# Kernel optimization log

Hardware: AMD Instinct MI355X
Metric: run time of the kernel (lower is better)

Reference implementation:

```python
import jax, jax.numpy as jnp
import numpy as np

E = 256   # embed_dim
L = 64    # num_landmarks
C = 256   # in_channels
N_ITER = 6


def iterative_inv(K):
    # Newton-Schulz pseudo-inverse on small [*, L, L] matrices (faithful to torch code)
    I = jnp.eye(K.shape[-1], dtype=K.dtype)
    KA = jnp.abs(K)
    V0 = KA.sum(axis=-2, keepdims=True).max(axis=-1, keepdims=True)  # [*,1,1]
    VI = KA.sum(axis=-1, keepdims=True).max(axis=-2, keepdims=True)  # [*,1,1]
    V = jnp.swapaxes(K, -1, -2) / (V0 * VI)
    for _ in range(N_ITER):
        KV = K @ V
        V = 0.25 * V @ (13.0 * I - KV @ (15.0 * I - KV @ (7.0 * I - KV)))
    return V


def setup_inputs() -> dict:
    key = jax.random.key(0)
    k0, k1, k2 = jax.random.split(key, 3)
    x = jax.random.normal(k0, (8, C, 64, 64), dtype=jnp.float32)
    # Conv2d 1x1 weights stored as [out, in]
    w_qkv = jax.random.normal(k1, (3 * E, C), dtype=jnp.float32) * 0.02
    b_qkv = jnp.zeros((3 * E,), dtype=jnp.float32)
    w_out = jax.random.normal(k2, (C, E), dtype=jnp.float32) * 0.02
    b_out = jnp.zeros((C,), dtype=jnp.float32)
    return {"x": x, "w_qkv": w_qkv, "b_qkv": b_qkv, "w_out": w_out, "b_out": b_out}


def reference(x, w_qkv, b_qkv, w_out, b_out):
    N, Cin, H, W = x.shape
    HW = H * W
    # 1x1 conv: [N, 3E, H, W]
    y = jnp.einsum('nchw,ec->nehw', x, w_qkv) + b_qkv[None, :, None, None]
    # faithful raw reshape (mixes channel/spatial like the torch code)
    qkv = y.reshape(N, HW, 3 * E)
    q, k, v = jnp.split(qkv, 3, axis=-1)                     # each [N, HW, E]
    scale = HW ** 0.5
    q_land = q.reshape(N, L, HW // L, E).mean(axis=-2) / scale  # [N, L, E]
    k_land = k.reshape(N, L, HW // L, E).mean(axis=-2) / scale  # [N, L, E]
    # three softmaxes, all over dim=-2 as in the original
    k1 = jax.nn.softmax(jnp.einsum('nie,nje->nij', q, k_land), axis=-2)       # [N, HW, L]
    k2 = jax.nn.softmax(jnp.einsum('nie,nje->nij', q_land, k_land), axis=-2)  # [N, L, L]
    k3 = jax.nn.softmax(jnp.einsum('nie,nje->nij', q_land, k), axis=-2)       # [N, L, HW]
    k2_inv = iterative_inv(k2)
    out = k1 @ (k2_inv @ (k3 @ v)) + v                        # [N, HW, E]
    out = out.reshape(N, E, H, W)                             # faithful raw reshape
    return jnp.einsum('nehw,ce->nchw', out, w_out) + b_out[None, :, None, None]
```

## Files before the change

kernel.cpp:

```cpp
#include <hip/hip_runtime.h>
#include <hip/hip_bf16.h>

typedef unsigned short u16;
typedef __attribute__((ext_vector_type(4))) float f32x4;
typedef __attribute__((ext_vector_type(8))) short short8;

#define NB   8
#define CIN  256
#define EDIM 256
#define M3   768
#define HWN  4096
#define LND  64
#define NS2  72

__device__ __forceinline__ float bf2f(u16 u){ return __uint_as_float(((unsigned)u)<<16); }
__device__ __forceinline__ u16 f2bf(float f){ __hip_bfloat16 h = __float2bfloat16(f); return *reinterpret_cast<u16*>(&h); }
__device__ __forceinline__ void bf2x2(unsigned u, float &lo, float &hi){
  lo = __uint_as_float(u<<16);
  hi = __uint_as_float(u & 0xffff0000u);
}

typedef __attribute__((address_space(1))) unsigned as1_uint;
typedef __attribute__((address_space(3))) unsigned as3_uint;
__device__ __forceinline__ void gl16(const void* g, void* l){
  __builtin_amdgcn_global_load_lds((const as1_uint*)g, (as3_uint*)l, 16, 0, 0);
}

__global__ __launch_bounds__(256) void k_prep(const float* __restrict__ x, u16* __restrict__ Xt,
                                              const float* __restrict__ wq, const float* __restrict__ wo,
                                              u16* __restrict__ Wqb, u16* __restrict__ Wob){
  const int bi = blockIdx.x;
  const int tid = threadIdx.x;
  if(bi >= 2048){
    int ti = (bi-2048)*256 + tid;
    const float* src; u16* dst;
    if(ti < 1536){ src = wq + (size_t)ti*128;        dst = Wqb + (size_t)ti*128; }
    else         { src = wo + (size_t)(ti-1536)*128; dst = Wob + (size_t)(ti-1536)*128; }
    #pragma unroll
    for(int t=0;t<128;t+=8){
      float4 v0 = *(const float4*)(src+t);
      float4 v1 = *(const float4*)(src+t+4);
      ushort4 o0, o1;
      o0.x=f2bf(v0.x); o0.y=f2bf(v0.y); o0.z=f2bf(v0.z); o0.w=f2bf(v0.w);
      o1.x=f2bf(v1.x); o1.y=f2bf(v1.y); o1.z=f2bf(v1.z); o1.w=f2bf(v1.w);
      *(ushort4*)(dst+t)   = o0;
      *(ushort4*)(dst+t+4) = o1;
    }
    return;
  }
  __shared__ float Ts[64*65];
  const int n = bi>>8, rem = bi&255, ct = rem>>6, pt = rem&63;
  const int c0 = ct*64, p0 = pt*64;
  {
    int cc = tid>>2, pj = (tid&3)*16;
    const float* xp = x + (size_t)n*CIN*HWN + (size_t)(c0+cc)*HWN + p0 + pj;
    #pragma unroll
    for(int j=0;j<16;j++) Ts[cc*65 + pj + j] = xp[j];
  }
  __syncthreads();
  {
    int pp = tid>>2, ej = (tid&3)*16;
    u16* op = Xt + ((size_t)n*HWN + p0 + pp)*CIN + c0 + ej;
    ushort4 o[4];
    #pragma unroll
    for(int j=0;j<16;j++) ((u16*)o)[j] = f2bf(Ts[(ej+j)*65 + pp]);
    *(ushort4*)(op+0)  = o[0];
    *(ushort4*)(op+4)  = o[1];
    *(ushort4*)(op+8)  = o[2];
    *(ushort4*)(op+12) = o[3];
  }
}

__global__ __launch_bounds__(256) void k_qkv(const u16* __restrict__ Wb, const u16* __restrict__ Xt,
                                             const float* __restrict__ bias, u16* __restrict__ Y){
  __shared__ __align__(16) u16 As[128*64];
  __shared__ __align__(16) u16 Bs[128*64];
  const int bi = blockIdx.x;
  const int n = bi&7, rem = bi>>3;
  const int ch0 = (rem%6)*128, p0 = (rem/6)*128;
  const int tid = threadIdx.x, lane = tid&63;
  const int c = tid&15, qq = (tid>>4)&3, w4 = tid>>6;
  const int wr0 = (w4&1)*64, wc0 = (w4>>1)*64;
  const u16* xb = Xt + ((size_t)n*HWN + p0)*CIN;
  const u16* wb = Wb + (size_t)ch0*CIN;
  f32x4 acc[4][4];
  #pragma unroll
  for(int mt=0;mt<4;mt++)
    #pragma unroll
    for(int nt=0;nt<4;nt++){ acc[mt][nt][0]=0.f; acc[mt][nt][1]=0.f; acc[mt][nt][2]=0.f; acc[mt][nt][3]=0.f; }
  const int srow  = w4*8 + (lane>>3);
  const int dslot = lane&7;
  const int sgo   = (dslot ^ (lane>>3))*8;
  const int rdswz = (c&7);
  for(int ph=0; ph<4; ph++){
    #pragma unroll
    for(int j=0;j<4;j++){
      int r = j*32 + srow;
      gl16(wb + (size_t)r*CIN + ph*64 + sgo, &As[r*64 + dslot*8]);
    }
    #pragma unroll
    for(int j=0;j<4;j++){
      int r = j*32 + srow;
      gl16(xb + (size_t)r*CIN + ph*64 + sgo, &Bs[r*64 + dslot*8]);
    }
    __syncthreads();
    #pragma unroll
    for(int kt=0;kt<2;kt++){
      short8 af[4], bff[4];
      const int rslot = ((kt*4+qq)^rdswz)*8;
      #pragma unroll
      for(int mt=0;mt<4;mt++) af[mt]  = *(const short8*)&As[(wr0+mt*16+c)*64 + rslot];
      #pragma unroll
      for(int nt=0;nt<4;nt++) bff[nt] = *(const short8*)&Bs[(wc0+nt*16+c)*64 + rslot];
      #pragma unroll
      for(int mt=0;mt<4;mt++)
        #pragma unroll
        for(int nt=0;nt<4;nt++)
          acc[mt][nt] = __builtin_amdgcn_mfma_f32_16x16x32_bf16(af[mt], bff[nt], acc[mt][nt], 0, 0, 0);
    }
    __syncthreads();
  }
  u16* Yb = Y + (size_t)n*M3*HWN;
  #pragma unroll
  for(int mt=0;mt<4;mt++){
    int chb = ch0 + wr0 + mt*16 + 4*qq;
    float b0 = bias[chb], b1 = bias[chb+1], b2 = bias[chb+2], b3 = bias[chb+3];
    #pragma unroll
    for(int nt=0;nt<4;nt++){
      int p = p0 + wc0 + nt*16 + c;
      u16* yp = Yb + (size_t)chb*HWN + p;
      yp[0]             = f2bf(acc[mt][nt][0]+b0);
      yp[HWN]           = f2bf(acc[mt][nt][1]+b1);
      yp[2*(size_t)HWN] = f2bf(acc[mt][nt][2]+b2);
      yp[3*(size_t)HWN] = f2bf(acc[mt][nt][3]+b3);
    }
  }
}

__global__ void k_land(const u16* __restrict__ Y, float* __restrict__ qland, float* __restrict__ kland){
  const int l = blockIdx.x, n = blockIdx.y, e = threadIdx.x;
  const u16* base = Y + (size_t)n*M3*HWN;
  float qs=0.f, ks=0.f;
  #pragma unroll 8
  for(int m=0;m<64;m++){
    size_t off = (size_t)(l*64+m)*M3;
    qs += bf2f(base[off+e]);
    ks += bf2f(base[off+256+e]);
  }
  qland[((size_t)n*LND+l)*EDIM+e] = qs*(1.f/4096.f);
  kland[((size_t)n*LND+l)*EDIM+e] = ks*(1.f/4096.f);
}

__device__ __forceinline__ void ns_mm2(const u16* L, int sL, const u16* Rt, int sR,
                                       int wv, int q, int c, f32x4 r4[4]){
  short8 a0 = *(const short8*)(L + (size_t)(16*wv + c)*sL + 8*q);
  short8 a1 = *(const short8*)(L + (size_t)(16*wv + c)*sL + 32 + 8*q);
  #pragma unroll
  for(int tc=0;tc<4;tc++){
    f32x4 acc = {0.f,0.f,0.f,0.f};
    short8 b0 = *(const short8*)(Rt + (size_t)(16*tc + c)*sR + 8*q);
    short8 b1 = *(const short8*)(Rt + (size_t)(16*tc + c)*sR + 32 + 8*q);
    acc = __builtin_amdgcn_mfma_f32_16x16x32_bf16(a0, b0, acc, 0, 0, 0);
    acc = __builtin_amdgcn_mfma_f32_16x16x32_bf16(a1, b1, acc, 0, 0, 0);
    r4[tc] = acc;
  }
}

#define TTS 64
__device__ void ns_body(int n, char* smem, const float* __restrict__ qland,
                        const float* __restrict__ kland, float* __restrict__ KinvT){
  u16* Kb  = (u16*)(smem + 0);
  u16* Vb  = (u16*)(smem + 9216);
  u16* Vt  = (u16*)(smem + 18432);
  u16* KVb = (u16*)(smem + 27648);
  u16* KVt = (u16*)(smem + 36864);
  u16* Tt  = (u16*)(smem + 46080);
  float* sS   = (float*)(smem + 27648);
  float* sred = (float*)(smem + 44544);
  const int tid = threadIdx.x;
  const int wv = tid>>6, q = (tid>>4)&3, c = tid&15;
  const float* qb = qland + (size_t)n*LND*EDIM;
  const float* kb = kland + (size_t)n*LND*EDIM;
  f32x4 acc[4];
  #pragma unroll
  for(int t=0;t<4;t++){ acc[t][0]=0.f; acc[t][1]=0.f; acc[t][2]=0.f; acc[t][3]=0.f; }
  for(int e0=0;e0<EDIM;e0+=64){
    __syncthreads();
    {
      int row = tid>>2, c0 = (tid&3)*16;
      const float* qp = qb + (size_t)row*EDIM + e0 + c0;
      const float* kp = kb + (size_t)row*EDIM + e0 + c0;
      u16* qd = &KVb[row*NS2 + c0];
      u16* kd = &KVt[row*NS2 + c0];
      #pragma unroll
      for(int j=0;j<16;j+=4){
        float4 qv = *(const float4*)(qp+j);
        float4 kv = *(const float4*)(kp+j);
        ushort4 qo, ko;
        qo.x=f2bf(qv.x); qo.y=f2bf(qv.y); qo.z=f2bf(qv.z); qo.w=f2bf(qv.w);
        ko.x=f2bf(kv.x); ko.y=f2bf(kv.y); ko.z=f2bf(kv.z); ko.w=f2bf(kv.w);
        *(ushort4*)(qd+j) = qo;
        *(ushort4*)(kd+j) = ko;
      }
    }
    __syncthreads();
    {
      short8 a0 = *(const short8*)&KVb[(16*wv+c)*NS2 + 8*q];
      short8 a1 = *(const short8*)&KVb[(16*wv+c)*NS2 + 32 + 8*q];
      #pragma unroll
      for(int tc=0;tc<4;tc++){
        short8 b0 = *(const short8*)&KVt[(16*tc+c)*NS2 + 8*q];
        short8 b1 = *(const short8*)&KVt[(16*tc+c)*NS2 + 32 + 8*q];
        acc[tc] = __builtin_amdgcn_mfma_f32_16x16x32_bf16(a0, b0, acc[tc], 0, 0, 0);
        acc[tc] = __builtin_amdgcn_mfma_f32_16x16x32_bf16(a1, b1, acc[tc], 0, 0, 0);
      }
    }
  }
  __syncthreads();
  #pragma unroll
  for(int tc=0;tc<4;tc++){
    int col = 16*tc + c, row0 = 16*wv + 4*q;
    sS[(row0+0)*66+col] = acc[tc][0];
    sS[(row0+1)*66+col] = acc[tc][1];
    sS[(row0+2)*66+col] = acc[tc][2];
    sS[(row0+3)*66+col] = acc[tc][3];
  }
  __syncthreads();
  if(tid < 64){
    int j = tid;
    float m = -1e30f;
    for(int i=0;i<64;i++) m = fmaxf(m, sS[i*66+j]);
    float ssum = 0.f;
    for(int i=0;i<64;i++) ssum += __expf(sS[i*66+j]-m);
    float inv = 1.f/ssum, cs = 0.f;
    for(int i=0;i<64;i++){
      float kv = __expf(sS[i*66+j]-m)*inv;
      cs += fabsf(kv);
      Kb[i*NS2+j] = f2bf(kv);
    }
    sred[j] = cs;
  }
  __syncthreads();
  if(tid < 64){
    int i = tid; float rs = 0.f;
    for(int j=0;j<64;j++) rs += fabsf(bf2f(Kb[i*NS2+j]));
    sred[64+i] = rs;
  }
  __syncthreads();
  if(tid == 0){
    float v0=-1e30f, vi=-1e30f;
    for(int t=0;t<64;t++){ v0 = fmaxf(v0, sred[t]); vi = fmaxf(vi, sred[64+t]); }
    sred[128] = 1.f/(v0*vi);
  }
  __syncthreads();
  {
    float sc = sred[128];
    int i = tid>>2, j16 = (tid&3)*16;
    #pragma unroll
    for(int jj=0;jj<16;jj++){
      int j = j16+jj;
      u16 bvv = f2bf(bf2f(Kb[j*NS2+i])*sc);
      Vb[i*NS2+j] = bvv;
      Vt[j*NS2+i] = bvv;
    }
  }
  __syncthreads();
  f32x4 r4[4];
  for(int it=0; it<6; it++){
    ns_mm2(Kb, NS2, Vt, NS2, wv, q, c, r4);
    #pragma unroll
    for(int tc=0;tc<4;tc++){
      int col = 16*tc + c, row0 = 16*wv + 4*q;
      ushort4 pk;
      pk.x = f2bf(r4[tc][0]); pk.y = f2bf(r4[tc][1]); pk.z = f2bf(r4[tc][2]); pk.w = f2bf(r4[tc][3]);
      KVb[(row0+0)*NS2+col] = pk.x; KVb[(row0+1)*NS2+col] = pk.y;
      KVb[(row0+2)*NS2+col] = pk.z; KVb[(row0+3)*NS2+col] = pk.w;
      *(ushort4*)&KVt[(size_t)col*NS2 + row0] = pk;
    }
    __syncthreads();
    ns_mm2(KVb, NS2, KVt, NS2, wv, q, c, r4);
    #pragma unroll
    for(int tc=0;tc<4;tc++){
      int col = 16*tc+c, row0 = 16*wv+4*q;
      ushort4 pk;
      #pragma unroll
      for(int r=0;r<4;r++){
        float kvv = bf2f(KVb[(row0+r)*NS2+col]);
        ((u16*)&pk)[r] = f2bf(7.f*kvv - r4[tc][r]);
      }
      *(ushort4*)&Tt[(size_t)col*TTS + row0] = pk;
    }
    __syncthreads();
    ns_mm2(KVb, NS2, Tt, TTS, wv, q, c, r4);
    __syncthreads();
    #pragma unroll
    for(int tc=0;tc<4;tc++){
      int col = 16*tc+c, row0 = 16*wv+4*q;
      ushort4 pk;
      #pragma unroll
      for(int r=0;r<4;r++){
        float kvv = bf2f(KVb[(row0+r)*NS2+col]);
        ((u16*)&pk)[r] = f2bf(15.f*kvv - r4[tc][r]);
      }
      *(ushort4*)&Tt[(size_t)col*TTS + row0] = pk;
    }
    __syncthreads();
    ns_mm2(Vb, NS2, Tt, TTS, wv, q, c, r4);
    __syncthreads();
    #pragma unroll
    for(int tc=0;tc<4;tc++){
      int col = 16*tc+c, row0 = 16*wv+4*q;
      float nv[4]; ushort4 pk;
      #pragma unroll
      for(int r=0;r<4;r++){
        float vv = bf2f(Vb[(row0+r)*NS2+col]);
        nv[r] = 0.25f*(13.f*vv - r4[tc][r]);
        u16 bb = f2bf(nv[r]);
        Vb[(row0+r)*NS2+col] = bb;
        ((u16*)&pk)[r] = bb;
      }
      *(ushort4*)&Vt[(size_t)col*NS2 + row0] = pk;
      if(it==5){
        *(float4*)&KinvT[(size_t)n*4096 + (size_t)col*64 + row0] = make_float4(nv[0],nv[1],nv[2],nv[3]);
      }
    }
    __syncthreads();
  }
}

#define LGS 264
__global__ __launch_bounds__(256) void k_landgemm(const u16* __restrict__ Y, const float* __restrict__ qland,
                                                  const float* __restrict__ kland, float* __restrict__ Z1,
                                                  float* __restrict__ Z3, float* __restrict__ KinvT){
  __shared__ __align__(16) char usm[54272];
  const int z = blockIdx.y;
  if(blockIdx.x == 64){
    if((z&1)==0) ns_body(z>>1, usm, qland, kland, KinvT);
    return;
  }
  u16* As = (u16*)usm;
  u16* BsU = (u16*)(usm + 33792);
  const int n = z>>1, which = z&1;
  const int b0 = blockIdx.x*64;
  const float* land = (which ? qland : kland) + (size_t)n*LND*EDIM;
  const int boff = which ? 256 : 0;
  float* out = (which ? Z3 : Z1) + (size_t)n*LND*HWN;
  const u16* Yb = Y + (size_t)n*M3*HWN + boff;
  const int tid = threadIdx.x, lane = tid&63;
  const int c = tid&15, qq = (tid>>4)&3, wv = tid>>6;
  {
    int r = tid>>2, c0 = (tid&3)*64;
    const float* lp = land + (size_t)r*EDIM + c0;
    u16* dp = &As[r*LGS + c0];
    #pragma unroll
    for(int j=0;j<64;j+=4){
      float4 v = *(const float4*)(lp+j);
      ushort4 o; o.x=f2bf(v.x); o.y=f2bf(v.y); o.z=f2bf(v.z); o.w=f2bf(v.w);
      *(ushort4*)(dp+j) = o;
    }
  }
  const int srow  = wv*8 + (lane>>3);
  const int dslot = lane&7;
  const int sgo   = (dslot ^ (lane>>3))*8;
  const int rdswz = (c&7);
  f32x4 acc[4];
  #pragma unroll
  for(int nt=0;nt<4;nt++){ acc[nt][0]=0.f; acc[nt][1]=0.f; acc[nt][2]=0.f; acc[nt][3]=0.f; }
  #pragma unroll
  for(int j=0;j<2;j++){
    int r = j*32 + srow;
    gl16(Yb + (size_t)(b0+r)*M3 + sgo, BsU + r*64 + dslot*8);
  }
  __syncthreads();
  for(int ph=0; ph<4; ph++){
    const int cur = ph&1;
    if(ph<3){
      #pragma unroll
      for(int j=0;j<2;j++){
        int r = j*32 + srow;
        gl16(Yb + (size_t)(b0+r)*M3 + (ph+1)*64 + sgo, BsU + (cur^1)*4096 + r*64 + dslot*8);
      }
    }
    #pragma unroll
    for(int kt=0;kt<2;kt++){
      short8 af = *(const short8*)&As[(16*wv + c)*LGS + ph*64 + kt*32 + qq*8];
      const int rslot = ((kt*4+qq)^rdswz)*8;
      #pragma unroll
      for(int nt=0;nt<4;nt++){
        short8 bff = *(const short8*)&BsU[cur*4096 + (nt*16+c)*64 + rslot];
        acc[nt] = __builtin_amdgcn_mfma_f32_16x16x32_bf16(af, bff, acc[nt], 0, 0, 0);
      }
    }
    __syncthreads();
  }
  const int m0 = 16*wv + 4*qq;
  #pragma unroll
  for(int nt=0;nt<4;nt++){
    int col = b0 + nt*16 + c;
    out[(size_t)(m0+0)*HWN + col] = acc[nt][0];
    out[(size_t)(m0+1)*HWN + col] = acc[nt][1];
    out[(size_t)(m0+2)*HWN + col] = acc[nt][2];
    out[(size_t)(m0+3)*HWN + col] = acc[nt][3];
  }
}

__device__ void soft3_body(int idx, char* smem, const float* __restrict__ Z3, u16* __restrict__ P){
  const int kc = idx&31, n = idx>>5;
  const int tid = threadIdx.x, jb = kc*128;
  float* Sf   = (float*)smem;
  float* sinv = (float*)(smem + 33792);
  const float* z3b = Z3 + (size_t)n*LND*HWN;
  {
    int ibase = (tid>>5)*8, j4 = (tid&31)*4;
    #pragma unroll
    for(int r=0;r<8;r++){
      int i = ibase + r;
      *(float4*)&Sf[i*132 + j4] = *(const float4*)&z3b[(size_t)i*HWN + jb + j4];
    }
  }
  __syncthreads();
  if(tid < 128){
    int j = tid;
    float m = -1e30f;
    for(int i=0;i<64;i++) m = fmaxf(m, Sf[i*132 + j]);
    float s = 0.f;
    for(int i=0;i<64;i++){ float e = __expf(Sf[i*132 + j] - m); Sf[i*132 + j] = e; s += e; }
    sinv[j] = 1.f/s;
  }
  __syncthreads();
  {
    int i = tid>>2, j0 = (tid&3)*32;
    u16* pp = P + ((size_t)n*LND + i)*HWN + jb + j0;
    #pragma unroll
    for(int t=0;t<32;t+=4){
      ushort4 o;
      o.x = f2bf(Sf[i*132 + j0+t+0]*sinv[j0+t+0]);
      o.y = f2bf(Sf[i*132 + j0+t+1]*sinv[j0+t+1]);
      o.z = f2bf(Sf[i*132 + j0+t+2]*sinv[j0+t+2]);
      o.w = f2bf(Sf[i*132 + j0+t+3]*sinv[j0+t+3]);
      *(ushort4*)(pp+t) = o;
    }
  }
}

__device__ void soft1_body(int b, char* smem, float* __restrict__ Z1){
  const int n = b>>6, j = b&63, tid = threadIdx.x;
  float* redm = (float*)smem;
  float* reds = redm + 4;
  float* base = Z1 + ((size_t)n*LND + j)*HWN;
  float v[16];
  float m = -1e30f;
  #pragma unroll
  for(int r=0;r<16;r++){ v[r] = base[r*256 + tid]; m = fmaxf(m, v[r]); }
  #pragma unroll
  for(int o=32;o;o>>=1) m = fmaxf(m, __shfl_xor(m, o));
  const int wid = tid>>6;
  if((tid&63)==0) redm[wid] = m;
  __syncthreads();
  m = fmaxf(fmaxf(redm[0],redm[1]), fmaxf(redm[2],redm[3]));
  float s = 0.f;
  #pragma unroll
  for(int r=0;r<16;r++){ v[r] = __expf(v[r]-m); s += v[r]; }
  #pragma unroll
  for(int o=32;o;o>>=1) s += __shfl_xor(s, o);
  if((tid&63)==0) reds[wid] = s;
  __syncthreads();
  s = reds[0]+reds[1]+reds[2]+reds[3];
  float inv = 1.f/s;
  #pragma unroll
  for(int r=0;r<16;r++) base[r*256 + tid] = v[r]*inv;
}

__global__ __launch_bounds__(256) void k_mega(const float* __restrict__ Z3, u16* __restrict__ P,
                                              float* __restrict__ Z1){
  __shared__ __align__(16) char smem[34304];
  const int bi = blockIdx.x;
  if(bi < 256) soft3_body(bi, smem, Z3, P);
  else         soft1_body(bi-256, smem, Z1);
}

__global__ __launch_bounds__(256) void k_pv(const u16* __restrict__ P, const u16* __restrict__ Y,
                                            float* __restrict__ part){
  __shared__ __align__(16) u16 As[64*64];
  __shared__ __align__(16) u16 Vt[128*64];
  const int bi = blockIdx.x;
  const int kc = bi&31, n = (bi>>5)&7, eh = bi>>8;
  const int jb = kc*128, eb = eh*128;
  const int tid = threadIdx.x, lane = tid&63;
  const int c = tid&15, qq = (tid>>4)&3, wv = tid>>6;
  const u16* Pb = P + (size_t)n*LND*HWN;
  const u16* Yb = Y + (size_t)n*M3*HWN;
  const int srow  = wv*8 + (lane>>3);
  const int dslot = lane&7;
  const int sgo   = (dslot ^ (lane>>3))*8;
  const int rdswz = (c&7);
  f32x4 acc[4][2];
  #pragma unroll
  for(int mt=0;mt<4;mt++)
    #pragma unroll
    for(int nt=0;nt<2;nt++){ acc[mt][nt][0]=0.f; acc[mt][nt][1]=0.f; acc[mt][nt][2]=0.f; acc[mt][nt][3]=0.f; }
  for(int ph=0; ph<2; ph++){
    #pragma unroll
    for(int j=0;j<2;j++){
      int r = j*32 + srow;
      gl16(Pb + (size_t)r*HWN + jb + ph*64 + sgo, &As[r*64 + dslot*8]);
    }
    #pragma unroll
    for(int rep=0; rep<4; rep++){
      int jl = (tid>>4) + 16*rep;
      int ec = (tid&15)*8;
      uint4 U = *(const uint4*)&Yb[(size_t)(jb+ph*64+jl)*M3 + 512 + eb + ec];
      const u16* uv = (const u16*)&U;
      #pragma unroll
      for(int k=0;k<8;k++){
        int e = ec+k;
        int slot = ((jl>>3) ^ (e&7) ^ ((e>>3)&7)) & 7;
        Vt[e*64 + slot*8 + (jl&7)] = uv[k];
      }
    }
    __syncthreads();
    #pragma unroll
    for(int kt=0;kt<2;kt++){
      const int rslotA = ((kt*4+qq)^rdswz)*8;
      short8 af[4];
      #pragma unroll
      for(int mt=0;mt<4;mt++) af[mt] = *(const short8*)&As[(mt*16+c)*64 + rslotA];
      #pragma unroll
      for(int nt=0;nt<2;nt++){
        int e = wv*32 + nt*16 + c;
        int slotB = ((kt*4+qq) ^ (e&7) ^ ((e>>3)&7)) & 7;
        short8 bf_ = *(const short8*)&Vt[e*64 + slotB*8];
        #pragma unroll
        for(int mt=0;mt<4;mt++)
          acc[mt][nt] = __builtin_amdgcn_mfma_f32_16x16x32_bf16(af[mt], bf_, acc[mt][nt], 0, 0, 0);
      }
    }
    __syncthreads();
  }
  float* pb = part + ((size_t)n*32 + kc)*LND*EDIM + eb;
  #pragma unroll
  for(int mt=0;mt<4;mt++){
    int row0 = mt*16 + 4*qq;
    #pragma unroll
    for(int nt=0;nt<2;nt++){
      int e = wv*32 + nt*16 + c;
      pb[(size_t)(row0+0)*EDIM + e] = acc[mt][nt][0];
      pb[(size_t)(row0+1)*EDIM + e] = acc[mt][nt][1];
      pb[(size_t)(row0+2)*EDIM + e] = acc[mt][nt][2];
      pb[(size_t)(row0+3)*EDIM + e] = acc[mt][nt][3];
    }
  }
}

__global__ __launch_bounds__(256) void k_c2(const float* __restrict__ KinvT, const float* __restrict__ part,
                                            u16* __restrict__ C2T){
  const int eb = blockIdx.x*64, n = blockIdx.y, tid = threadIdx.x;
  __shared__ float KT[64][68];
  __shared__ float Bs2[64][68];
  __shared__ u16 Ct[64*72];
  {
    int l = tid>>2, o16 = (tid&3)*16;
    const float* kp = KinvT + (size_t)n*4096 + l*64 + o16;
    #pragma unroll
    for(int t=0;t<16;t+=4) *(float4*)&KT[l][o16+t] = *(const float4*)(kp+t);
    const float* pp = part + (size_t)n*32*16384 + (size_t)l*256 + eb + o16;
    float4 s0 = {0,0,0,0}, s1 = {0,0,0,0}, s2 = {0,0,0,0}, s3 = {0,0,0,0};
    for(int kc=0;kc<32;kc++){
      const float* b = pp + (size_t)kc*16384;
      float4 v0 = *(const float4*)(b);
      float4 v1 = *(const float4*)(b+4);
      float4 v2 = *(const float4*)(b+8);
      float4 v3 = *(const float4*)(b+12);
      s0.x+=v0.x; s0.y+=v0.y; s0.z+=v0.z; s0.w+=v0.w;
      s1.x+=v1.x; s1.y+=v1.y; s1.z+=v1.z; s1.w+=v1.w;
      s2.x+=v2.x; s2.y+=v2.y; s2.z+=v2.z; s2.w+=v2.w;
      s3.x+=v3.x; s3.y+=v3.y; s3.z+=v3.z; s3.w+=v3.w;
    }
    *(float4*)&Bs2[l][o16+0]  = s0;
    *(float4*)&Bs2[l][o16+4]  = s1;
    *(float4*)&Bs2[l][o16+8]  = s2;
    *(float4*)&Bs2[l][o16+12] = s3;
  }
  __syncthreads();
  const int j0 = (tid>>4)*4, u0 = (tid&15)*4;
  float acc[4][4] = {};
  #pragma unroll 8
  for(int l=0;l<64;l++){
    f32x4 a = *(f32x4*)&KT[l][j0];
    f32x4 b = *(f32x4*)&Bs2[l][u0];
    #pragma unroll
    for(int s=0;s<4;s++)
      #pragma unroll
      for(int u=0;u<4;u++) acc[s][u] += a[s]*b[u];
  }
  #pragma unroll
  for(int s=0;s<4;s++)
    #pragma unroll
    for(int u=0;u<4;u++)
      Ct[(u0+u)*72 + j0+s] = f2bf(acc[s][u]);
  __syncthreads();
  {
    int e = tid>>2, j16 = (tid&3)*16;
    u16* op = C2T + ((size_t)n*256 + eb + e)*64 + j16;
    #pragma unroll
    for(int t=0;t<16;t+=4)
      *(ushort4*)(op+t) = *(const ushort4*)&Ct[e*72 + j16 + t];
  }
}

__global__ __launch_bounds__(256) void k_out(const float* __restrict__ Z1, const u16* __restrict__ C2T,
                                             const u16* __restrict__ Y, u16* __restrict__ OM){
  __shared__ __align__(16) u16 Cs[256*64];
  __shared__ __align__(16) u16 Zt[64*72];
  const int ib = blockIdx.x*64, n = blockIdx.y;
  const int tid = threadIdx.x, lane = tid&63;
  const int c = tid&15, qq = (tid>>4)&3, wv = tid>>6;
  const int srow  = wv*8 + (lane>>3);
  const int dslot = lane&7;
  const int sgo   = (dslot ^ (lane>>3))*8;
  const int rdswz = (c&7);
  const u16* cb = C2T + (size_t)n*256*64;
  #pragma unroll
  for(int j=0;j<8;j++){
    int r = j*32 + srow;
    gl16(cb + (size_t)r*64 + sgo, &Cs[r*64 + dslot*8]);
  }
  {
    int j = tid>>2, i16 = (tid&3)*16;
    const float* zp = Z1 + ((size_t)n*LND + j)*HWN + ib + i16;
    #pragma unroll
    for(int t=0;t<16;t+=4){
      float4 v = *(const float4*)(zp+t);
      Zt[(i16+t+0)*72 + j] = f2bf(v.x);
      Zt[(i16+t+1)*72 + j] = f2bf(v.y);
      Zt[(i16+t+2)*72 + j] = f2bf(v.z);
      Zt[(i16+t+3)*72 + j] = f2bf(v.w);
    }
  }
  __syncthreads();
  f32x4 acc[4][4];
  #pragma unroll
  for(int mt=0;mt<4;mt++)
    #pragma unroll
    for(int nt=0;nt<4;nt++){ acc[mt][nt][0]=0.f; acc[mt][nt][1]=0.f; acc[mt][nt][2]=0.f; acc[mt][nt][3]=0.f; }
  #pragma unroll
  for(int kt=0;kt<2;kt++){
    const int rslot = ((kt*4+qq)^rdswz)*8;
    short8 af[4], bf_[4];
    #pragma unroll
    for(int mt=0;mt<4;mt++) af[mt] = *(const short8*)&Cs[(wv*64+mt*16+c)*64 + rslot];
    #pragma unroll
    for(int nt=0;nt<4;nt++) bf_[nt] = *(const short8*)&Zt[(nt*16+c)*72 + kt*32 + qq*8];
    #pragma unroll
    for(int mt=0;mt<4;mt++)
      #pragma unroll
      for(int nt=0;nt<4;nt++)
        acc[mt][nt] = __builtin_amdgcn_mfma_f32_16x16x32_bf16(af[mt], bf_[nt], acc[mt][nt], 0, 0, 0);
  }
  const u16* Yb = Y + (size_t)n*M3*HWN;
  u16* ob = OM + (size_t)n*HWN*EDIM;
  #pragma unroll
  for(int mt=0;mt<4;mt++){
    int e = wv*64 + mt*16 + 4*qq;
    #pragma unroll
    for(int nt=0;nt<4;nt++){
      int i = ib + nt*16 + c;
      ushort4 V4 = *(const ushort4*)(Yb + (size_t)i*M3 + 512 + e);
      ushort4 o;
      o.x = f2bf(acc[mt][nt][0] + bf2f(V4.x));
      o.y = f2bf(acc[mt][nt][1] + bf2f(V4.y));
      o.z = f2bf(acc[mt][nt][2] + bf2f(V4.z));
      o.w = f2bf(acc[mt][nt][3] + bf2f(V4.w));
      *(ushort4*)(ob + (size_t)i*EDIM + e) = o;
    }
  }
}

__global__ __launch_bounds__(256) void k_proj(const u16* __restrict__ Wb, const u16* __restrict__ OM,
                                              const float* __restrict__ bias, float* __restrict__ out){
  __shared__ __align__(16) u16 As[128*64];
  __shared__ __align__(16) u16 Bt[128*64];
  const int bi = blockIdx.x;
  const int n = bi&7, rem = bi>>3;
  const int ch0 = (rem&1)*128, p0 = (rem>>1)*128;
  const int tid = threadIdx.x, lane = tid&63;
  const int c = tid&15, qq = (tid>>4)&3, w4 = tid>>6;
  const int wr0 = (w4&1)*64, wc0 = (w4>>1)*64;
  const u16* omb = OM + (size_t)n*HWN*EDIM;
  const u16* wb = Wb + (size_t)ch0*EDIM;
  f32x4 acc[4][4];
  #pragma unroll
  for(int mt=0;mt<4;mt++)
    #pragma unroll
    for(int nt=0;nt<4;nt++){ acc[mt][nt][0]=0.f; acc[mt][nt][1]=0.f; acc[mt][nt][2]=0.f; acc[mt][nt][3]=0.f; }
  const int srow  = w4*8 + (lane>>3);
  const int dslot = lane&7;
  const int sgo   = (dslot ^ (lane>>3))*8;
  const int rdswz = (c&7);
  for(int ph=0; ph<4; ph++){
    #pragma unroll
    for(int j=0;j<4;j++){
      int r = j*32 + srow;
      gl16(wb + (size_t)r*EDIM + ph*64 + sgo, &As[r*64 + dslot*8]);
    }
    #pragma unroll
    for(int rep=0; rep<4; rep++){
      int ee = (tid>>4) + 16*rep;
      int pc = (tid&15)*8;
      uint4 U = *(const uint4*)&omb[(size_t)(ph*64+ee)*HWN + p0 + pc];
      const u16* uv = (const u16*)&U;
      #pragma unroll
      for(int k=0;k<8;k++){
        int p = pc+k;
        int slot = ((ee>>3) ^ (p&7) ^ ((p>>3)&7)) & 7;
        Bt[p*64 + slot*8 + (ee&7)] = uv[k];
      }
    }
    __syncthreads();
    #pragma unroll
    for(int kt=0;kt<2;kt++){
      const int rslot = ((kt*4+qq)^rdswz)*8;
      short8 af[4], bff[4];
      #pragma unroll
      for(int mt=0;mt<4;mt++) af[mt] = *(const short8*)&As[(wr0+mt*16+c)*64 + rslot];
      #pragma unroll
      for(int nt=0;nt<4;nt++){
        int p = wc0 + nt*16 + c;
        int slotB = ((kt*4+qq) ^ (p&7) ^ ((p>>3)&7)) & 7;
        bff[nt] = *(const short8*)&Bt[p*64 + slotB*8];
      }
      #pragma unroll
      for(int mt=0;mt<4;mt++)
        #pragma unroll
        for(int nt=0;nt<4;nt++)
          acc[mt][nt] = __builtin_amdgcn_mfma_f32_16x16x32_bf16(af[mt], bff[nt], acc[mt][nt], 0, 0, 0);
    }
    __syncthreads();
  }
  float* ob = out + (size_t)n*EDIM*HWN;
  #pragma unroll
  for(int mt=0;mt<4;mt++){
    int chb = ch0 + wr0 + mt*16 + 4*qq;
    float b0 = bias[chb], b1 = bias[chb+1], b2 = bias[chb+2], b3 = bias[chb+3];
    #pragma unroll
    for(int nt=0;nt<4;nt++){
      int p = p0 + wc0 + nt*16 + c;
      float* yp = ob + (size_t)chb*HWN + p;
      yp[0]             = acc[mt][nt][0]+b0;
      yp[HWN]           = acc[mt][nt][1]+b1;
      yp[2*(size_t)HWN] = acc[mt][nt][2]+b2;
      yp[3*(size_t)HWN] = acc[mt][nt][3]+b3;
    }
  }
}

extern "C" void kernel_launch(void* const* d_in, const int* in_sizes, int n_in,
                              void* d_out, int out_size, void* d_ws, size_t ws_size,
                              hipStream_t stream){
  (void)out_size; (void)ws_size;
  const float* x     = (const float*)d_in[0];
  const float* w_qkv = (const float*)d_in[1];
  const float* b_qkv = (const float*)d_in[2];
  const float* w_out = (const float*)d_in[3];
  const float* b_out = (const float*)d_in[4];
  for(int i=0;i<n_in;i++){
    switch(in_sizes[i]){
      case 8388608: x     = (const float*)d_in[i]; break;
      case 196608:  w_qkv = (const float*)d_in[i]; break;
      case 768:     b_qkv = (const float*)d_in[i]; break;
      case 65536:   w_out = (const float*)d_in[i]; break;
      case 256:     b_out = (const float*)d_in[i]; break;
      default: break;
    }
  }
  float* out = (float*)d_out;
  char* ws = (char*)d_ws;

  u16*   Y     = (u16*)(ws + 0);
  float* qland = (float*)(ws + 50331648);
  float* kland = (float*)(ws + 50855936);
  float* Z1    = (float*)(ws + 51380224);
  float* Z3    = (float*)(ws + 59768832);
  float* KinvT = (float*)(ws + 68157440);
  float* part  = (float*)(ws + 68288512);
  u16*   Xt    = (u16*)(ws + 68288512);
  u16*   C2T   = (u16*)(ws + 85065728);
  u16*   OM    = (u16*)(ws + 86114304);
  u16*   Pbuf  = (u16*)(ws + 86114304);
  u16*   Wqb   = (u16*)(ws + 59768832);
  u16*   Wob   = (u16*)(ws + 102891520);

  k_prep    <<<dim3(2056),   256, 0, stream>>>(x, Xt, w_qkv, w_out, Wqb, Wob);
  k_qkv     <<<dim3(1536),   256, 0, stream>>>(Wqb, Xt, b_qkv, Y);
  k_land    <<<dim3(64,8),   256, 0, stream>>>(Y, qland, kland);
  k_landgemm<<<dim3(65,16),  256, 0, stream>>>(Y, qland, kland, Z1, Z3, KinvT);
  k_mega    <<<dim3(768),    256, 0, stream>>>(Z3, Pbuf, Z1);
  k_pv      <<<dim3(512),    256, 0, stream>>>(Pbuf, Y, part);
  k_c2      <<<dim3(4,8),    256, 0, stream>>>(KinvT, part, C2T);
  k_out     <<<dim3(64,8),   256, 0, stream>>>(Z1, C2T, Y, OM);
  k_proj    <<<dim3(512),    256, 0, stream>>>(Wob, OM, b_out, out);
}
```

Before: 211.5 us.

## Fuse column softmax of Z3 into PV GEMM kernel, drop P buffer

The column-softmax over landmark logits Z3 moves into the k_pv kernel. Each block computes its softmax tile in shared memory and writes the bf16 probabilities straight into a swizzled LDS A-operand buffer, instead of round-tripping them through global memory. The soft1 softmax blocks are appended to the same launch, which removes one kernel launch and the P write and read traffic. In exchange, each softmax tile is now computed twice (once per E-half block), and LDS use per block grows to about 50KB, which may lower occupancy.

```diff
diff --git a/kernel.cpp b/kernel.cpp
--- a/kernel.cpp
+++ b/kernel.cpp
@@ -404,11 +404,48 @@
   }
 }
 
-__device__ void soft3_body(int idx, char* smem, const float* __restrict__ Z3, u16* __restrict__ P){
-  const int kc = idx&31, n = idx>>5;
-  const int tid = threadIdx.x, jb = kc*128;
+__device__ void soft1_body(int b, char* smem, float* __restrict__ Z1){
+  const int n = b>>6, j = b&63, tid = threadIdx.x;
+  float* redm = (float*)smem;
+  float* reds = redm + 4;
+  float* base = Z1 + ((size_t)n*LND + j)*HWN;
+  float v[16];
+  float m = -1e30f;
+  #pragma unroll
+  for(int r=0;r<16;r++){ v[r] = base[r*256 + tid]; m = fmaxf(m, v[r]); }
+  #pragma unroll
+  for(int o=32;o;o>>=1) m = fmaxf(m, __shfl_xor(m, o));
+  const int wid = tid>>6;
+  if((tid&63)==0) redm[wid] = m;
+  __syncthreads();
+  m = fmaxf(fmaxf(redm[0],redm[1]), fmaxf(redm[2],redm[3]));
+  float s = 0.f;
+  #pragma unroll
+  for(int r=0;r<16;r++){ v[r] = __expf(v[r]-m); s += v[r]; }
+  #pragma unroll
+  for(int o=32;o;o>>=1) s += __shfl_xor(s, o);
+  if((tid&63)==0) reds[wid] = s;
+  __syncthreads();
+  s = reds[0]+reds[1]+reds[2]+reds[3];
+  float inv = 1.f/s;
+  #pragma unroll
+  for(int r=0;r<16;r++) base[r*256 + tid] = v[r]*inv;
+}
+
+__global__ __launch_bounds__(256) void k_pv(const float* __restrict__ Z3, const u16* __restrict__ Y,
+                                            float* __restrict__ part, float* __restrict__ Z1){
+  __shared__ __align__(16) char smem[50688];
+  const int bi = blockIdx.x;
+  if(bi >= 512){ soft1_body(bi-512, smem, Z1); return; }
   float* Sf   = (float*)smem;
   float* sinv = (float*)(smem + 33792);
+  u16*   Asb  = (u16*)(smem + 34304);
+  u16*   Vt   = (u16*)smem;
+  const int kc = bi&31, n = (bi>>5)&7, eh = bi>>8;
+  const int jb = kc*128, eb = eh*128;
+  const int tid = threadIdx.x, lane = tid&63;
+  const int c = tid&15, qq = (tid>>4)&3, wv = tid>>6;
+  const u16* Yb = Y + (size_t)n*M3*HWN;
   const float* z3b = Z3 + (size_t)n*LND*HWN;
   {
     int ibase = (tid>>5)*8, j4 = (tid&31)*4;
@@ -429,70 +466,21 @@
   }
   __syncthreads();
   {
-    int i = tid>>2, j0 = (tid&3)*32;
-    u16* pp = P + ((size_t)n*LND + i)*HWN + jb + j0;
+    int i = tid>>2, j0q = (tid&3)*32;
+    const int iswz = (i&7);
     #pragma unroll
     for(int t=0;t<32;t+=4){
+      int jg = j0q + t;
+      int phb = jg>>6, jl = jg&63;
       ushort4 o;
-      o.x = f2bf(Sf[i*132 + j0+t+0]*sinv[j0+t+0]);
-      o.y = f2bf(Sf[i*132 + j0+t+1]*sinv[j0+t+1]);
-      o.z = f2bf(Sf[i*132 + j0+t+2]*sinv[j0+t+2]);
-      o.w = f2bf(Sf[i*132 + j0+t+3]*sinv[j0+t+3]);
-      *(ushort4*)(pp+t) = o;
-    }
-  }
-}
-
-__device__ void soft1_body(int b, char* smem, float* __restrict__ Z1){
-  const int n = b>>6, j = b&63, tid = threadIdx.x;
-  float* redm = (float*)smem;
-  float* reds = redm + 4;
-  float* base = Z1 + ((size_t)n*LND + j)*HWN;
-  float v[16];
-  float m = -1e30f;
-  #pragma unroll
-  for(int r=0;r<16;r++){ v[r] = base[r*256 + tid]; m = fmaxf(m, v[r]); }
-  #pragma unroll
-  for(int o=32;o;o>>=1) m = fmaxf(m, __shfl_xor(m, o));
-  const int wid = tid>>6;
-  if((tid&63)==0) redm[wid] = m;
-  __syncthreads();
-  m = fmaxf(fmaxf(redm[0],redm[1]), fmaxf(redm[2],redm[3]));
-  float s = 0.f;
-  #pragma unroll
-  for(int r=0;r<16;r++){ v[r] = __expf(v[r]-m); s += v[r]; }
-  #pragma unroll
-  for(int o=32;o;o>>=1) s += __shfl_xor(s, o);
-  if((tid&63)==0) reds[wid] = s;
-  __syncthreads();
-  s = reds[0]+reds[1]+reds[2]+reds[3];
-  float inv = 1.f/s;
-  #pragma unroll
-  for(int r=0;r<16;r++) base[r*256 + tid] = v[r]*inv;
-}
-
-__global__ __launch_bounds__(256) void k_mega(const float* __restrict__ Z3, u16* __restrict__ P,
-                                              float* __restrict__ Z1){
-  __shared__ __align__(16) char smem[34304];
-  const int bi = blockIdx.x;
-  if(bi < 256) soft3_body(bi, smem, Z3, P);
-  else         soft1_body(bi-256, smem, Z1);
-}
-
-__global__ __launch_bounds__(256) void k_pv(const u16* __restrict__ P, const u16* __restrict__ Y,
-                                            float* __restrict__ part){
-  __shared__ __align__(16) u16 As[64*64];
-  __shared__ __align__(16) u16 Vt[128*64];
-  const int bi = blockIdx.x;
-  const int kc = bi&31, n = (bi>>5)&7, eh = bi>>8;
-  const int jb = kc*128, eb = eh*128;
-  const int tid = threadIdx.x, lane = tid&63;
-  const int c = tid&15, qq = (tid>>4)&3, wv = tid>>6;
-  const u16* Pb = P + (size_t)n*LND*HWN;
-  const u16* Yb = Y + (size_t)n*M3*HWN;
-  const int srow  = wv*8 + (lane>>3);
-  const int dslot = lane&7;
-  const int sgo   = (dslot ^ (lane>>3))*8;
+      o.x = f2bf(Sf[i*132 + jg+0]*sinv[jg+0]);
+      o.y = f2bf(Sf[i*132 + jg+1]*sinv[jg+1]);
+      o.z = f2bf(Sf[i*132 + jg+2]*sinv[jg+2]);
+      o.w = f2bf(Sf[i*132 + jg+3]*sinv[jg+3]);
+      *(ushort4*)&Asb[phb*4096 + i*64 + ((jl>>3)^iswz)*8 + (jl&7)] = o;
+    }
+  }
+  __syncthreads();
   const int rdswz = (c&7);
   f32x4 acc[4][2];
   #pragma unroll
@@ -500,11 +488,6 @@
     #pragma unroll
     for(int nt=0;nt<2;nt++){ acc[mt][nt][0]=0.f; acc[mt][nt][1]=0.f; acc[mt][nt][2]=0.f; acc[mt][nt][3]=0.f; }
   for(int ph=0; ph<2; ph++){
-    #pragma unroll
-    for(int j=0;j<2;j++){
-      int r = j*32 + srow;
-      gl16(Pb + (size_t)r*HWN + jb + ph*64 + sgo, &As[r*64 + dslot*8]);
-    }
     #pragma unroll
     for(int rep=0; rep<4; rep++){
       int jl = (tid>>4) + 16*rep;
@@ -524,7 +507,7 @@
       const int rslotA = ((kt*4+qq)^rdswz)*8;
       short8 af[4];
       #pragma unroll
-      for(int mt=0;mt<4;mt++) af[mt] = *(const short8*)&As[(mt*16+c)*64 + rslotA];
+      for(int mt=0;mt<4;mt++) af[mt] = *(const short8*)&Asb[ph*4096 + (mt*16+c)*64 + rslotA];
       #pragma unroll
       for(int nt=0;nt<2;nt++){
         int e = wv*32 + nt*16 + c;
@@ -786,7 +769,6 @@
   u16*   Xt    = (u16*)(ws + 68288512);
   u16*   C2T   = (u16*)(ws + 85065728);
   u16*   OM    = (u16*)(ws + 86114304);
-  u16*   Pbuf  = (u16*)(ws + 86114304);
   u16*   Wqb   = (u16*)(ws + 59768832);
   u16*   Wob   = (u16*)(ws + 102891520);
 
@@ -794,8 +776,7 @@
   k_qkv     <<<dim3(1536),   256, 0, stream>>>(Wqb, Xt, b_qkv, Y);
   k_land    <<<dim3(64,8),   256, 0, stream>>>(Y, qland, kland);
   k_landgemm<<<dim3(65,16),  256, 0, stream>>>(Y, qland, kland, Z1, Z3, KinvT);
-  k_mega    <<<dim3(768),    256, 0, stream>>>(Z3, Pbuf, Z1);
-  k_pv      <<<dim3(512),    256, 0, stream>>>(Pbuf, Y, part);
+  k_pv      <<<dim3(1024),   256, 0, stream>>>(Z3, Y, part, Z1);
   k_c2      <<<dim3(4,8),    256, 0, stream>>>(KinvT, part, C2T);
   k_out     <<<dim3(64,8),   256, 0, stream>>>(Z1, C2T, Y, OM);
   k_proj    <<<dim3(512),    256, 0, stream>>>(Wob, OM, b_out, out);
```

New measurement: 202.5 us. 4.3% less time.
